# Performance work log

Hardware: AMD Instinct MI355X
Metric: run time of the kernel (lower is better)

The kernel has to match this reference:

```python
import jax, jax.numpy as jnp
import numpy as np

N, E, G = 50000, 400000, 64
IN_CH, HID, H, EDGE_DIM = 128, 64, 4, 4
NEG_SLOPE = 0.2


def setup_inputs() -> dict:
    key = jax.random.key(0)
    ks = list(jax.random.split(key, 40))
    kit = iter(ks)

    def rn(shape, scale=0.05):
        return jax.random.normal(next(kit), shape, dtype=jnp.float32) * scale

    inp = {
        "x": jax.random.normal(next(kit), (N, IN_CH), dtype=jnp.float32),
        "edge_attr": jax.random.uniform(next(kit), (E, 2), dtype=jnp.float32),
        "edge_index": jax.random.randint(next(kit), (2, E), 0, N),
        "batch": jnp.sort(jax.random.randint(next(kit), (N,), 0, G)),
    }
    # edge feature fusion MLPs
    inp["W_et"] = rn((1, EDGE_DIM // 2)); inp["b_et"] = jnp.zeros((EDGE_DIM // 2,), jnp.float32)
    inp["W_uw"] = rn((1, EDGE_DIM // 2)); inp["b_uw"] = jnp.zeros((EDGE_DIM // 2,), jnp.float32)
    inp["W_ua"] = rn((1, 1));             inp["b_ua"] = jnp.zeros((1,), jnp.float32)
    # two GATv2 layers
    for li, ic in ((0, IN_CH), (1, HID)):
        inp[f"Wl{li}"] = rn((ic, H * HID)); inp[f"bl{li}"] = jnp.zeros((H * HID,), jnp.float32)
        inp[f"Wr{li}"] = rn((ic, H * HID)); inp[f"br{li}"] = jnp.zeros((H * HID,), jnp.float32)
        inp[f"att{li}"] = rn((H, HID))
        inp[f"We{li}"] = rn((EDGE_DIM, H * HID))
        inp[f"bias{li}"] = jnp.zeros((HID,), jnp.float32)
    # heads
    inp["W_fc"] = rn((HID, HID)); inp["b_fc"] = jnp.zeros((HID,), jnp.float32)
    inp["W_res"] = rn((HID, 1)); inp["b_res"] = jnp.zeros((1,), jnp.float32)
    inp["W_time"] = rn((HID, 1)); inp["b_time"] = jnp.zeros((1,), jnp.float32)
    return inp


def gatv2_layer(x, src, dst, edge_attr_proj, Wl, bl, Wr, br, att, We, bias):
    # GATv2Conv, concat=False (mean over heads)
    xl = (x @ Wl + bl).reshape(-1, H, HID)   # [N,H,C] transformed source feats
    xr = (x @ Wr + br).reshape(-1, H, HID)   # [N,H,C] transformed target feats
    ee = (edge_attr_proj @ We).reshape(-1, H, HID)  # [E,H,C]
    xj = xl[src]                              # per-edge gather of source
    m = jax.nn.leaky_relu(xj + xr[dst] + ee, NEG_SLOPE)  # [E,H,C]
    score = jnp.einsum('ehc,hc->eh', m, att)  # [E,H]
    # segment softmax over incoming edges of each destination node
    smax = jax.ops.segment_max(score, dst, num_segments=N)  # [N,H]
    ex = jnp.exp(score - smax[dst])
    denom = jax.ops.segment_sum(ex, dst, num_segments=N)
    alpha = ex / (denom[dst] + 1e-16)         # [E,H]
    out = jax.ops.segment_sum(xj * alpha[..., None], dst, num_segments=N)  # [N,H,C]
    return out.mean(axis=1) + bias            # [N,C]


def reference(x, edge_attr, W_et, b_et, W_uw, b_uw, W_ua, b_ua,
              Wl0, bl0, Wr0, br0, att0, We0, bias0,
              Wl1, bl1, Wr1, br1, att1, We1, bias1,
              W_fc, b_fc, W_res, b_res, W_time, b_time,
              edge_index, batch):
    src, dst = edge_index[0], edge_index[1]
    edge_type = edge_attr[:, 0:1]
    unwind = edge_attr[:, 1:2]
    et_emb = edge_type @ W_et + b_et
    uw_emb = unwind @ W_uw + b_uw
    uw_att = jax.nn.sigmoid(unwind @ W_ua + b_ua)
    eap = jnp.concatenate([et_emb, uw_emb * uw_att], axis=-1)  # [E,4]

    h = jax.nn.relu(gatv2_layer(x, src, dst, eap, Wl0, bl0, Wr0, br0, att0, We0, bias0))
    h = jax.nn.relu(gatv2_layer(h, src, dst, eap, Wl1, bl1, Wr1, br1, att1, We1, bias1))

    # global mean pool over graphs (dropout is identity at inference)
    sums = jax.ops.segment_sum(h, batch, num_segments=G)
    cnts = jax.ops.segment_sum(jnp.ones((h.shape[0],), h.dtype), batch, num_segments=G)
    pooled = sums / jnp.maximum(cnts, 1.0)[:, None]
    g = jax.nn.relu(pooled @ W_fc + b_fc)
    result = g @ W_res + b_res
    time = g @ W_time + b_time
    return jnp.concatenate([result, time], axis=1)  # [G,2]
```

## Files before the change

kernel.cpp:

```cpp
#include <hip/hip_runtime.h>
#include <math.h>

namespace {

constexpr int N = 50000;
constexpr int E = 400000;
constexpr int G = 64;
constexpr int HID = 64;
constexpr int HH = 256;
constexpr int NCT = 32;
constexpr float NEG = 0.2f;

typedef __attribute__((ext_vector_type(8))) short short8v;
typedef __attribute__((ext_vector_type(4))) float f32x4;

__device__ __forceinline__ unsigned short f2bf(float f) {
    unsigned int u = __float_as_uint(f);
    u += 0x7FFFu + ((u >> 16) & 1u);
    return (unsigned short)(u >> 16);
}
__device__ __forceinline__ float bf2f(unsigned short h) {
    return __uint_as_float(((unsigned int)h) << 16);
}

__global__ __launch_bounds__(256) void hist_k(
    const int* __restrict__ dst, int* __restrict__ deg, int* __restrict__ rank)
{
    int e = blockIdx.x * 256 + threadIdx.x;
    if (e < E) rank[e] = atomicAdd(&deg[dst[e]], 1);
}

__global__ __launch_bounds__(256) void scan1_k(
    const int* __restrict__ deg, int* __restrict__ pre, int* __restrict__ bsum)
{
    __shared__ int s[256];
    int i = blockIdx.x * 256 + threadIdx.x;
    int v = (i < N) ? deg[i] : 0;
    s[threadIdx.x] = v;
    __syncthreads();
    for (int off = 1; off < 256; off <<= 1) {
        int t = (threadIdx.x >= off) ? s[threadIdx.x - off] : 0;
        __syncthreads();
        s[threadIdx.x] += t;
        __syncthreads();
    }
    if (i < N) pre[i] = s[threadIdx.x] - v;
    if (threadIdx.x == 255) bsum[blockIdx.x] = s[255];
}

__global__ __launch_bounds__(256) void scan2_k(int* __restrict__ bsum, int nb)
{
    __shared__ int s[256];
    int tid = threadIdx.x;
    int v = (tid < nb) ? bsum[tid] : 0;
    s[tid] = v;
    __syncthreads();
    for (int off = 1; off < 256; off <<= 1) {
        int t = (tid >= off) ? s[tid - off] : 0;
        __syncthreads();
        s[tid] += t;
        __syncthreads();
    }
    if (tid < nb) bsum[tid] = s[tid] - v;
}

__global__ __launch_bounds__(256) void scatter_k(
    const int* __restrict__ src, const int* __restrict__ dst,
    const float* __restrict__ ea,
    const float* __restrict__ W_et, const float* __restrict__ b_et,
    const float* __restrict__ W_uw, const float* __restrict__ b_uw,
    const float* __restrict__ W_ua, const float* __restrict__ b_ua,
    const int* __restrict__ pre, const int* __restrict__ bsum,
    const int* __restrict__ rank,
    int* __restrict__ csr_src, float* __restrict__ eap_csr)
{
    int e = blockIdx.x * 256 + threadIdx.x;
    if (e >= E) return;
    float et = ea[e * 2 + 0], uw = ea[e * 2 + 1];
    float ua = 1.f / (1.f + expf(-(uw * W_ua[0] + b_ua[0])));
    float4 v;
    v.x = et * W_et[0] + b_et[0];
    v.y = et * W_et[1] + b_et[1];
    v.z = (uw * W_uw[0] + b_uw[0]) * ua;
    v.w = (uw * W_uw[1] + b_uw[1]) * ua;
    int d = dst[e];
    int pos = pre[d] + bsum[d >> 8] + rank[e];
    csr_src[pos] = src[e];
    *(float4*)&eap_csr[(size_t)pos * 4] = v;
}

__global__ __launch_bounds__(256) void pack_k(
    const float* __restrict__ Wl0, const float* __restrict__ Wr0,
    const float* __restrict__ bl0, const float* __restrict__ br0,
    const float* __restrict__ Wl1, const float* __restrict__ Wr1,
    const float* __restrict__ bl1, const float* __restrict__ br1,
    unsigned short* __restrict__ w0hi, unsigned short* __restrict__ w0lo,
    unsigned short* __restrict__ w1hi, unsigned short* __restrict__ w1lo,
    float* __restrict__ bc0, float* __restrict__ bc1)
{
    int idx = blockIdx.x * 256 + threadIdx.x;
    if (idx < 8192) {
        int lane = idx & 63, ct = (idx >> 6) & 31, kt = idx >> 11;
        int col = ct * 16 + (lane & 15);
        const float* W = (col < 256) ? Wl0 : Wr0;
        int c = col & 255;
        int kb = kt * 32 + ((lane >> 4) & 3) * 8;
#pragma unroll
        for (int e = 0; e < 8; e++) {
            float v = W[(size_t)(kb + e) * 256 + c];
            unsigned short hi = f2bf(v);
            unsigned short lo = f2bf(v - bf2f(hi));
            w0hi[(size_t)idx * 8 + e] = hi;
            w0lo[(size_t)idx * 8 + e] = lo;
        }
    } else if (idx < 8192 + 4096) {
        int s = idx - 8192;
        int lane = s & 63, ct = (s >> 6) & 31, kt = s >> 11;
        int col = ct * 16 + (lane & 15);
        const float* W = (col < 256) ? Wl1 : Wr1;
        int c = col & 255;
        int kb = kt * 32 + ((lane >> 4) & 3) * 8;
#pragma unroll
        for (int e = 0; e < 8; e++) {
            float v = W[(size_t)(kb + e) * 256 + c];
            unsigned short hi = f2bf(v);
            unsigned short lo = f2bf(v - bf2f(hi));
            w1hi[(size_t)s * 8 + e] = hi;
            w1lo[(size_t)s * 8 + e] = lo;
        }
    } else if (idx < 8192 + 4096 + 512) {
        int i = idx - (8192 + 4096);
        bc0[i] = (i < 256) ? bl0[i] : br0[i - 256];
    } else if (idx < 8192 + 4096 + 1024) {
        int i = idx - (8192 + 4096 + 512);
        bc1[i] = (i < 256) ? bl1[i] : br1[i - 256];
    }
}

template <int IC>
__global__ __launch_bounds__(256) void projmm_k(
    const float* __restrict__ x,
    const unsigned short* __restrict__ whi, const unsigned short* __restrict__ wlo,
    const float* __restrict__ bc,
    float* __restrict__ xl, float* __restrict__ xr)
{
    constexpr int KT = IC / 32;
    constexpr int LDX = IC + 4;
    __shared__ float xs[32][LDX];
    const int base = blockIdx.x * 32;
    const int tid = threadIdx.x;
    for (int idx = tid; idx < 32 * IC / 4; idx += 256) {
        int j = idx / (IC / 4), k4 = idx - j * (IC / 4);
        int n = base + j;
        float4 v = make_float4(0.f, 0.f, 0.f, 0.f);
        if (n < N) v = *(const float4*)&x[(size_t)n * IC + k4 * 4];
        *(float4*)&xs[j][k4 * 4] = v;
    }
    __syncthreads();
    const int w = tid >> 6, lane = tid & 63;
    const int lr = lane & 15, lg = lane >> 4;
    f32x4 acc[2][8];
#pragma unroll
    for (int rt = 0; rt < 2; rt++)
#pragma unroll
        for (int ct = 0; ct < 8; ct++) {
            f32x4 z = {0.f, 0.f, 0.f, 0.f};
            acc[rt][ct] = z;
        }
#pragma unroll
    for (int kt = 0; kt < KT; kt++) {
        short8v ahi[2], alo[2];
#pragma unroll
        for (int rt = 0; rt < 2; rt++) {
            const float* p = &xs[rt * 16 + lr][kt * 32 + lg * 8];
            float4 v0 = *(const float4*)p;
            float4 v1 = *(const float4*)(p + 4);
            float fv[8] = {v0.x, v0.y, v0.z, v0.w, v1.x, v1.y, v1.z, v1.w};
            short8v h, l;
#pragma unroll
            for (int e = 0; e < 8; e++) {
                unsigned short hb = f2bf(fv[e]);
                h[e] = (short)hb;
                l[e] = (short)f2bf(fv[e] - bf2f(hb));
            }
            ahi[rt] = h;
            alo[rt] = l;
        }
        const size_t bbase = ((size_t)(kt * NCT + w * 8) * 64 + lane) * 8;
#pragma unroll
        for (int ct = 0; ct < 8; ct++) {
            short8v bhi = *(const short8v*)&whi[bbase + (size_t)ct * 64 * 8];
            short8v blo = *(const short8v*)&wlo[bbase + (size_t)ct * 64 * 8];
#pragma unroll
            for (int rt = 0; rt < 2; rt++) {
                acc[rt][ct] = __builtin_amdgcn_mfma_f32_16x16x32_bf16(ahi[rt], bhi, acc[rt][ct], 0, 0, 0);
                acc[rt][ct] = __builtin_amdgcn_mfma_f32_16x16x32_bf16(alo[rt], bhi, acc[rt][ct], 0, 0, 0);
                acc[rt][ct] = __builtin_amdgcn_mfma_f32_16x16x32_bf16(ahi[rt], blo, acc[rt][ct], 0, 0, 0);
            }
        }
    }
#pragma unroll
    for (int ct = 0; ct < 8; ct++) {
        int col = (w * 8 + ct) * 16 + lr;
        float bv = bc[col];
        float* target;
        int c;
        if (col < 256) { target = xl; c = col; }
        else           { target = xr; c = col - 256; }
#pragma unroll
        for (int rt = 0; rt < 2; rt++) {
            int row0 = base + rt * 16 + lg * 4;
            f32x4 a = acc[rt][ct];
#pragma unroll
            for (int i = 0; i < 4; i++) {
                int r = row0 + i;
                if (r < N) target[(size_t)r * HH + c] = a[i] + bv;
            }
        }
    }
}

__global__ __launch_bounds__(256) void gat_aggr_k(
    const float* __restrict__ xl, const float* __restrict__ xr,
    const float* __restrict__ eap_csr, const float* __restrict__ We,
    const float* __restrict__ att,
    const int* __restrict__ pre, const int* __restrict__ bsum,
    const int* __restrict__ deg,
    const int* __restrict__ csr_src,
    const float* __restrict__ bias, float* __restrict__ hout)
{
    int d = blockIdx.x * 4 + (threadIdx.x >> 6);
    int lane = threadIdx.x & 63;
    if (d >= N) return;
    int c4 = lane * 4;
    const float4 w0 = *(const float4*)&We[0 * HH + c4];
    const float4 w1 = *(const float4*)&We[1 * HH + c4];
    const float4 w2 = *(const float4*)&We[2 * HH + c4];
    const float4 w3 = *(const float4*)&We[3 * HH + c4];
    const float4 av = *(const float4*)&att[c4];
    const float4 vr = *(const float4*)&xr[(size_t)d * HH + c4];
    int start = pre[d] + bsum[d >> 8];
    int end = start + deg[d];
    float m = -INFINITY, denom = 0.f;
    float ax = 0.f, ay = 0.f, az = 0.f, aw = 0.f;
    int idx = start;
    for (; idx + 4 <= end; idx += 4) {
        int s0 = csr_src[idx], s1 = csr_src[idx + 1];
        int s2 = csr_src[idx + 2], s3 = csr_src[idx + 3];
        float4 a0 = *(const float4*)&eap_csr[(size_t)(idx + 0) * 4];
        float4 a1 = *(const float4*)&eap_csr[(size_t)(idx + 1) * 4];
        float4 a2 = *(const float4*)&eap_csr[(size_t)(idx + 2) * 4];
        float4 a3 = *(const float4*)&eap_csr[(size_t)(idx + 3) * 4];
        float4 vl0 = *(const float4*)&xl[(size_t)s0 * HH + c4];
        float4 vl1 = *(const float4*)&xl[(size_t)s1 * HH + c4];
        float4 vl2 = *(const float4*)&xl[(size_t)s2 * HH + c4];
        float4 vl3 = *(const float4*)&xl[(size_t)s3 * HH + c4];
        float p0, p1, p2, p3;
        {
            float q0 = vl0.x + vr.x + a0.x * w0.x + a0.y * w1.x + a0.z * w2.x + a0.w * w3.x;
            float q1 = vl0.y + vr.y + a0.x * w0.y + a0.y * w1.y + a0.z * w2.y + a0.w * w3.y;
            float q2 = vl0.z + vr.z + a0.x * w0.z + a0.y * w1.z + a0.z * w2.z + a0.w * w3.z;
            float q3 = vl0.w + vr.w + a0.x * w0.w + a0.y * w1.w + a0.z * w2.w + a0.w * w3.w;
            q0 = (q0 > 0.f) ? q0 : NEG * q0; q1 = (q1 > 0.f) ? q1 : NEG * q1;
            q2 = (q2 > 0.f) ? q2 : NEG * q2; q3 = (q3 > 0.f) ? q3 : NEG * q3;
            p0 = q0 * av.x + q1 * av.y + q2 * av.z + q3 * av.w;
        }
        {
            float q0 = vl1.x + vr.x + a1.x * w0.x + a1.y * w1.x + a1.z * w2.x + a1.w * w3.x;
            float q1 = vl1.y + vr.y + a1.x * w0.y + a1.y * w1.y + a1.z * w2.y + a1.w * w3.y;
            float q2 = vl1.z + vr.z + a1.x * w0.z + a1.y * w1.z + a1.z * w2.z + a1.w * w3.z;
            float q3 = vl1.w + vr.w + a1.x * w0.w + a1.y * w1.w + a1.z * w2.w + a1.w * w3.w;
            q0 = (q0 > 0.f) ? q0 : NEG * q0; q1 = (q1 > 0.f) ? q1 : NEG * q1;
            q2 = (q2 > 0.f) ? q2 : NEG * q2; q3 = (q3 > 0.f) ? q3 : NEG * q3;
            p1 = q0 * av.x + q1 * av.y + q2 * av.z + q3 * av.w;
        }
        {
            float q0 = vl2.x + vr.x + a2.x * w0.x + a2.y * w1.x + a2.z * w2.x + a2.w * w3.x;
            float q1 = vl2.y + vr.y + a2.x * w0.y + a2.y * w1.y + a2.z * w2.y + a2.w * w3.y;
            float q2 = vl2.z + vr.z + a2.x * w0.z + a2.y * w1.z + a2.z * w2.z + a2.w * w3.z;
            float q3 = vl2.w + vr.w + a2.x * w0.w + a2.y * w1.w + a2.z * w2.w + a2.w * w3.w;
            q0 = (q0 > 0.f) ? q0 : NEG * q0; q1 = (q1 > 0.f) ? q1 : NEG * q1;
            q2 = (q2 > 0.f) ? q2 : NEG * q2; q3 = (q3 > 0.f) ? q3 : NEG * q3;
            p2 = q0 * av.x + q1 * av.y + q2 * av.z + q3 * av.w;
        }
        {
            float q0 = vl3.x + vr.x + a3.x * w0.x + a3.y * w1.x + a3.z * w2.x + a3.w * w3.x;
            float q1 = vl3.y + vr.y + a3.x * w0.y + a3.y * w1.y + a3.z * w2.y + a3.w * w3.y;
            float q2 = vl3.z + vr.z + a3.x * w0.z + a3.y * w1.z + a3.z * w2.z + a3.w * w3.z;
            float q3 = vl3.w + vr.w + a3.x * w0.w + a3.y * w1.w + a3.z * w2.w + a3.w * w3.w;
            q0 = (q0 > 0.f) ? q0 : NEG * q0; q1 = (q1 > 0.f) ? q1 : NEG * q1;
            q2 = (q2 > 0.f) ? q2 : NEG * q2; q3 = (q3 > 0.f) ? q3 : NEG * q3;
            p3 = q0 * av.x + q1 * av.y + q2 * av.z + q3 * av.w;
        }
#pragma unroll
        for (int off = 1; off <= 8; off <<= 1) {
            p0 += __shfl_xor(p0, off, 64);
            p1 += __shfl_xor(p1, off, 64);
            p2 += __shfl_xor(p2, off, 64);
            p3 += __shfl_xor(p3, off, 64);
        }
        float pm = fmaxf(fmaxf(p0, p1), fmaxf(p2, p3));
        float newm = fmaxf(m, pm);
        float so = expf(m - newm);
        float e0 = expf(p0 - newm);
        float e1 = expf(p1 - newm);
        float e2 = expf(p2 - newm);
        float e3 = expf(p3 - newm);
        denom = denom * so + e0 + e1 + e2 + e3;
        ax = ax * so + e0 * vl0.x + e1 * vl1.x + e2 * vl2.x + e3 * vl3.x;
        ay = ay * so + e0 * vl0.y + e1 * vl1.y + e2 * vl2.y + e3 * vl3.y;
        az = az * so + e0 * vl0.z + e1 * vl1.z + e2 * vl2.z + e3 * vl3.z;
        aw = aw * so + e0 * vl0.w + e1 * vl1.w + e2 * vl2.w + e3 * vl3.w;
        m = newm;
    }
    for (; idx < end; ++idx) {
        int s = csr_src[idx];
        float4 a = *(const float4*)&eap_csr[(size_t)idx * 4];
        float4 vl = *(const float4*)&xl[(size_t)s * HH + c4];
        float q0 = vl.x + vr.x + a.x * w0.x + a.y * w1.x + a.z * w2.x + a.w * w3.x;
        float q1 = vl.y + vr.y + a.x * w0.y + a.y * w1.y + a.z * w2.y + a.w * w3.y;
        float q2 = vl.z + vr.z + a.x * w0.z + a.y * w1.z + a.z * w2.z + a.w * w3.z;
        float q3 = vl.w + vr.w + a.x * w0.w + a.y * w1.w + a.z * w2.w + a.w * w3.w;
        q0 = (q0 > 0.f) ? q0 : NEG * q0; q1 = (q1 > 0.f) ? q1 : NEG * q1;
        q2 = (q2 > 0.f) ? q2 : NEG * q2; q3 = (q3 > 0.f) ? q3 : NEG * q3;
        float p = q0 * av.x + q1 * av.y + q2 * av.z + q3 * av.w;
#pragma unroll
        for (int off = 1; off <= 8; off <<= 1) p += __shfl_xor(p, off, 64);
        float newm = fmaxf(m, p);
        float so = expf(m - newm);
        float ex = expf(p - newm);
        denom = denom * so + ex;
        ax = ax * so + ex * vl.x;
        ay = ay * so + ex * vl.y;
        az = az * so + ex * vl.z;
        aw = aw * so + ex * vl.w;
        m = newm;
    }
    float inv = 0.25f / (denom + 1e-16f);
    ax *= inv; ay *= inv; az *= inv; aw *= inv;
    ax += __shfl_xor(ax, 16, 64); ax += __shfl_xor(ax, 32, 64);
    ay += __shfl_xor(ay, 16, 64); ay += __shfl_xor(ay, 32, 64);
    az += __shfl_xor(az, 16, 64); az += __shfl_xor(az, 32, 64);
    aw += __shfl_xor(aw, 16, 64); aw += __shfl_xor(aw, 32, 64);
    if (lane < 16) {
        float4 b = *(const float4*)&bias[c4];
        float4 o;
        o.x = fmaxf(ax + b.x, 0.f);
        o.y = fmaxf(ay + b.y, 0.f);
        o.z = fmaxf(az + b.z, 0.f);
        o.w = fmaxf(aw + b.w, 0.f);
        *(float4*)&hout[(size_t)d * HID + c4] = o;
    }
}

__global__ __launch_bounds__(256) void pool_k(
    const float* __restrict__ h, const int* __restrict__ batch,
    float* __restrict__ pooled)
{
    constexpr int CH = 16;
    int c = threadIdx.x & 63;
    int chunk = blockIdx.x * 4 + (threadIdx.x >> 6);
    int n0 = chunk * CH;
    if (n0 >= N) return;
    int nend = (n0 + CH < N) ? n0 + CH : N;
    float sum = 0.f;
    int curb = batch[n0];
    for (int n = n0; n < nend; ++n) {
        int b = batch[n];
        if (b != curb) {
            atomicAdd(&pooled[curb * HID + c], sum);
            sum = 0.f; curb = b;
        }
        sum += h[(size_t)n * HID + c];
    }
    atomicAdd(&pooled[curb * HID + c], sum);
}

__global__ __launch_bounds__(64) void head_k(
    const float* __restrict__ pooled, const int* __restrict__ batch,
    const float* __restrict__ W_fc, const float* __restrict__ b_fc,
    const float* __restrict__ W_res, const float* __restrict__ b_res,
    const float* __restrict__ W_time, const float* __restrict__ b_time,
    float* __restrict__ out)
{
    int g = blockIdx.x;
    int c = threadIdx.x;
    int lo = 0, hi = N;
    while (lo < hi) { int mid = (lo + hi) >> 1; if (batch[mid] < g) lo = mid + 1; else hi = mid; }
    int start = lo;
    hi = N;
    while (lo < hi) { int mid = (lo + hi) >> 1; if (batch[mid] < g + 1) lo = mid + 1; else hi = mid; }
    int end = lo;
    float cnt = (float)(end - start);
    float p = pooled[g * HID + c] / fmaxf(cnt, 1.0f);
    __shared__ float ps[HID];
    ps[c] = p;
    __syncthreads();
    float gv = b_fc[c];
    for (int k = 0; k < HID; k++) gv += ps[k] * W_fc[k * HID + c];
    gv = fmaxf(gv, 0.f);
    float r = gv * W_res[c];
    float t = gv * W_time[c];
#pragma unroll
    for (int off = 32; off > 0; off >>= 1) {
        r += __shfl_down(r, off, 64);
        t += __shfl_down(t, off, 64);
    }
    if (c == 0) {
        out[g * 2 + 0] = r + b_res[0];
        out[g * 2 + 1] = t + b_time[0];
    }
}

}

extern "C" void kernel_launch(void* const* d_in, const int* in_sizes, int n_in,
                              void* d_out, int out_size, void* d_ws, size_t ws_size,
                              hipStream_t stream) {
    const float* x         = (const float*)d_in[0];
    const float* edge_attr = (const float*)d_in[1];
    const int*   edge_index= (const int*)d_in[2];
    const int*   batch     = (const int*)d_in[3];
    const float* W_et = (const float*)d_in[4];
    const float* b_et = (const float*)d_in[5];
    const float* W_uw = (const float*)d_in[6];
    const float* b_uw = (const float*)d_in[7];
    const float* W_ua = (const float*)d_in[8];
    const float* b_ua = (const float*)d_in[9];
    const float* Wl0  = (const float*)d_in[10];
    const float* bl0  = (const float*)d_in[11];
    const float* Wr0  = (const float*)d_in[12];
    const float* br0  = (const float*)d_in[13];
    const float* att0 = (const float*)d_in[14];
    const float* We0  = (const float*)d_in[15];
    const float* bias0= (const float*)d_in[16];
    const float* Wl1  = (const float*)d_in[17];
    const float* bl1  = (const float*)d_in[18];
    const float* Wr1  = (const float*)d_in[19];
    const float* br1  = (const float*)d_in[20];
    const float* att1 = (const float*)d_in[21];
    const float* We1  = (const float*)d_in[22];
    const float* bias1= (const float*)d_in[23];
    const float* W_fc = (const float*)d_in[24];
    const float* b_fc = (const float*)d_in[25];
    const float* W_res= (const float*)d_in[26];
    const float* b_res= (const float*)d_in[27];
    const float* W_time=(const float*)d_in[28];
    const float* b_time=(const float*)d_in[29];

    const int* src = edge_index;
    const int* dst = edge_index + E;

    float* ws    = (float*)d_ws;
    float* xl    = ws;
    float* xr    = xl  + (size_t)N * HH;
    float* h1    = xr  + (size_t)N * HH;
    float* h2    = h1  + (size_t)N * HID;
    float* pooled= h2  + (size_t)N * HID;
    int*   deg      = (int*)(pooled + (size_t)G * HID);
    int*   pre      = deg + N;
    int*   bsum     = pre + N;
    int*   rank     = bsum + 256;
    int*   csr_src  = rank + E;
    float* eap_csr  = (float*)(csr_src + E);
    unsigned short* w0hi = (unsigned short*)rank;
    unsigned short* w0lo = w0hi + 65536;
    unsigned short* w1hi = w0lo + 65536;
    unsigned short* w1lo = w1hi + 32768;
    float* bc0 = (float*)(w1lo + 32768);
    float* bc1 = bc0 + 512;

    dim3 b256(256);
    const int NB = (N + 255) / 256;
    const int NPROJ = (N + 31) / 32;

    hipMemsetAsync(pooled, 0, (size_t)(G * HID + N) * 4, stream);
    hist_k<<<(E + 255) / 256, b256, 0, stream>>>(dst, deg, rank);
    scan1_k<<<NB, b256, 0, stream>>>(deg, pre, bsum);
    scan2_k<<<1, b256, 0, stream>>>(bsum, NB);
    scatter_k<<<(E + 255) / 256, b256, 0, stream>>>(
        src, dst, edge_attr, W_et, b_et, W_uw, b_uw, W_ua, b_ua,
        pre, bsum, rank, csr_src, eap_csr);
    pack_k<<<52, b256, 0, stream>>>(Wl0, Wr0, bl0, br0, Wl1, Wr1, bl1, br1,
                                    w0hi, w0lo, w1hi, w1lo, bc0, bc1);

    projmm_k<128><<<NPROJ, b256, 0, stream>>>(x, w0hi, w0lo, bc0, xl, xr);
    gat_aggr_k<<<(N + 3) / 4, b256, 0, stream>>>(
        xl, xr, eap_csr, We0, att0, pre, bsum, deg, csr_src, bias0, h1);

    projmm_k<64><<<NPROJ, b256, 0, stream>>>(h1, w1hi, w1lo, bc1, xl, xr);
    gat_aggr_k<<<(N + 3) / 4, b256, 0, stream>>>(
        xl, xr, eap_csr, We1, att1, pre, bsum, deg, csr_src, bias1, h2);

    pool_k<<<((N + 15) / 16 + 3) / 4, b256, 0, stream>>>(h2, batch, pooled);
    head_k<<<G, dim3(64), 0, stream>>>(
        pooled, batch, W_fc, b_fc, W_res, b_res, W_time, b_time, (float*)d_out);
}
```

Before: 421.0 us.

## Store projected features as bf16 and use persistent atomic work queue in aggregation

```diff
diff --git a/kernel.cpp b/kernel.cpp
--- a/kernel.cpp
+++ b/kernel.cpp
@@ -10,6 +10,7 @@
 constexpr int HH = 256;
 constexpr int NCT = 32;
 constexpr float NEG = 0.2f;
+constexpr int GAT_BLOCKS = 2048;
 
 typedef __attribute__((ext_vector_type(8))) short short8v;
 typedef __attribute__((ext_vector_type(4))) float f32x4;
@@ -21,6 +22,15 @@
 }
 __device__ __forceinline__ float bf2f(unsigned short h) {
     return __uint_as_float(((unsigned int)h) << 16);
+}
+__device__ __forceinline__ float4 ld_bf4(const unsigned short* p) {
+    uint2 u = *(const uint2*)p;
+    float4 r;
+    r.x = __uint_as_float(u.x << 16);
+    r.y = __uint_as_float(u.x & 0xFFFF0000u);
+    r.z = __uint_as_float(u.y << 16);
+    r.w = __uint_as_float(u.y & 0xFFFF0000u);
+    return r;
 }
 
 __global__ __launch_bounds__(256) void hist_k(
@@ -96,9 +106,11 @@
     const float* __restrict__ bl1, const float* __restrict__ br1,
     unsigned short* __restrict__ w0hi, unsigned short* __restrict__ w0lo,
     unsigned short* __restrict__ w1hi, unsigned short* __restrict__ w1lo,
-    float* __restrict__ bc0, float* __restrict__ bc1)
+    float* __restrict__ bc0, float* __restrict__ bc1,
+    int* __restrict__ ctr)
 {
     int idx = blockIdx.x * 256 + threadIdx.x;
+    if (idx == 0) { ctr[0] = 0; ctr[1] = 0; }
     if (idx < 8192) {
         int lane = idx & 63, ct = (idx >> 6) & 31, kt = idx >> 11;
         int col = ct * 16 + (lane & 15);
@@ -142,7 +154,7 @@
     const float* __restrict__ x,
     const unsigned short* __restrict__ whi, const unsigned short* __restrict__ wlo,
     const float* __restrict__ bc,
-    float* __restrict__ xl, float* __restrict__ xr)
+    unsigned short* __restrict__ xlb, unsigned short* __restrict__ xrb)
 {
     constexpr int KT = IC / 32;
     constexpr int LDX = IC + 4;
@@ -203,10 +215,10 @@
     for (int ct = 0; ct < 8; ct++) {
         int col = (w * 8 + ct) * 16 + lr;
         float bv = bc[col];
-        float* target;
+        unsigned short* target;
         int c;
-        if (col < 256) { target = xl; c = col; }
-        else           { target = xr; c = col - 256; }
+        if (col < 256) { target = xlb; c = col; }
+        else           { target = xrb; c = col - 256; }
 #pragma unroll
         for (int rt = 0; rt < 2; rt++) {
             int row0 = base + rt * 16 + lg * 4;
@@ -214,142 +226,152 @@
 #pragma unroll
             for (int i = 0; i < 4; i++) {
                 int r = row0 + i;
-                if (r < N) target[(size_t)r * HH + c] = a[i] + bv;
+                if (r < N) target[(size_t)r * HH + c] = f2bf(a[i] + bv);
             }
         }
     }
 }
 
 __global__ __launch_bounds__(256) void gat_aggr_k(
-    const float* __restrict__ xl, const float* __restrict__ xr,
+    const unsigned short* __restrict__ xlb, const unsigned short* __restrict__ xrb,
     const float* __restrict__ eap_csr, const float* __restrict__ We,
     const float* __restrict__ att,
     const int* __restrict__ pre, const int* __restrict__ bsum,
     const int* __restrict__ deg,
     const int* __restrict__ csr_src,
-    const float* __restrict__ bias, float* __restrict__ hout)
-{
-    int d = blockIdx.x * 4 + (threadIdx.x >> 6);
-    int lane = threadIdx.x & 63;
-    if (d >= N) return;
-    int c4 = lane * 4;
+    const float* __restrict__ bias, float* __restrict__ hout,
+    int* __restrict__ ctr)
+{
+    const int lane = threadIdx.x & 63;
+    const int c4 = lane * 4;
     const float4 w0 = *(const float4*)&We[0 * HH + c4];
     const float4 w1 = *(const float4*)&We[1 * HH + c4];
     const float4 w2 = *(const float4*)&We[2 * HH + c4];
     const float4 w3 = *(const float4*)&We[3 * HH + c4];
     const float4 av = *(const float4*)&att[c4];
-    const float4 vr = *(const float4*)&xr[(size_t)d * HH + c4];
-    int start = pre[d] + bsum[d >> 8];
-    int end = start + deg[d];
-    float m = -INFINITY, denom = 0.f;
-    float ax = 0.f, ay = 0.f, az = 0.f, aw = 0.f;
-    int idx = start;
-    for (; idx + 4 <= end; idx += 4) {
-        int s0 = csr_src[idx], s1 = csr_src[idx + 1];
-        int s2 = csr_src[idx + 2], s3 = csr_src[idx + 3];
-        float4 a0 = *(const float4*)&eap_csr[(size_t)(idx + 0) * 4];
-        float4 a1 = *(const float4*)&eap_csr[(size_t)(idx + 1) * 4];
-        float4 a2 = *(const float4*)&eap_csr[(size_t)(idx + 2) * 4];
-        float4 a3 = *(const float4*)&eap_csr[(size_t)(idx + 3) * 4];
-        float4 vl0 = *(const float4*)&xl[(size_t)s0 * HH + c4];
-        float4 vl1 = *(const float4*)&xl[(size_t)s1 * HH + c4];
-        float4 vl2 = *(const float4*)&xl[(size_t)s2 * HH + c4];
-        float4 vl3 = *(const float4*)&xl[(size_t)s3 * HH + c4];
-        float p0, p1, p2, p3;
-        {
-            float q0 = vl0.x + vr.x + a0.x * w0.x + a0.y * w1.x + a0.z * w2.x + a0.w * w3.x;
-            float q1 = vl0.y + vr.y + a0.x * w0.y + a0.y * w1.y + a0.z * w2.y + a0.w * w3.y;
-            float q2 = vl0.z + vr.z + a0.x * w0.z + a0.y * w1.z + a0.z * w2.z + a0.w * w3.z;
-            float q3 = vl0.w + vr.w + a0.x * w0.w + a0.y * w1.w + a0.z * w2.w + a0.w * w3.w;
+    float4 bb = make_float4(0.f, 0.f, 0.f, 0.f);
+    if (lane < 16) bb = *(const float4*)&bias[c4];
+
+    int draw = 0;
+    if (lane == 0) draw = atomicAdd(ctr, 1);
+    int d = __builtin_amdgcn_readfirstlane(draw);
+    while (d < N) {
+        int dnraw = 0;
+        if (lane == 0) dnraw = atomicAdd(ctr, 1);
+
+        int start = pre[d] + bsum[d >> 8];
+        int end = start + deg[d];
+        const float4 vr = ld_bf4(&xrb[(size_t)d * HH + c4]);
+        float m = -INFINITY, denom = 0.f;
+        float ax = 0.f, ay = 0.f, az = 0.f, aw = 0.f;
+        int idx = start;
+        for (; idx + 4 <= end; idx += 4) {
+            int s0 = csr_src[idx], s1 = csr_src[idx + 1];
+            int s2 = csr_src[idx + 2], s3 = csr_src[idx + 3];
+            float4 a0 = *(const float4*)&eap_csr[(size_t)(idx + 0) * 4];
+            float4 a1 = *(const float4*)&eap_csr[(size_t)(idx + 1) * 4];
+            float4 a2 = *(const float4*)&eap_csr[(size_t)(idx + 2) * 4];
+            float4 a3 = *(const float4*)&eap_csr[(size_t)(idx + 3) * 4];
+            float4 vl0 = ld_bf4(&xlb[(size_t)s0 * HH + c4]);
+            float4 vl1 = ld_bf4(&xlb[(size_t)s1 * HH + c4]);
+            float4 vl2 = ld_bf4(&xlb[(size_t)s2 * HH + c4]);
+            float4 vl3 = ld_bf4(&xlb[(size_t)s3 * HH + c4]);
+            float p0, p1, p2, p3;
+            {
+                float q0 = vl0.x + vr.x + a0.x * w0.x + a0.y * w1.x + a0.z * w2.x + a0.w * w3.x;
+                float q1 = vl0.y + vr.y + a0.x * w0.y + a0.y * w1.y + a0.z * w2.y + a0.w * w3.y;
+                float q2 = vl0.z + vr.z + a0.x * w0.z + a0.y * w1.z + a0.z * w2.z + a0.w * w3.z;
+                float q3 = vl0.w + vr.w + a0.x * w0.w + a0.y * w1.w + a0.z * w2.w + a0.w * w3.w;
+                q0 = (q0 > 0.f) ? q0 : NEG * q0; q1 = (q1 > 0.f) ? q1 : NEG * q1;
+                q2 = (q2 > 0.f) ? q2 : NEG * q2; q3 = (q3 > 0.f) ? q3 : NEG * q3;
+                p0 = q0 * av.x + q1 * av.y + q2 * av.z + q3 * av.w;
+            }
+            {
+                float q0 = vl1.x + vr.x + a1.x * w0.x + a1.y * w1.x + a1.z * w2.x + a1.w * w3.x;
+                float q1 = vl1.y + vr.y + a1.x * w0.y + a1.y * w1.y + a1.z * w2.y + a1.w * w3.y;
+                float q2 = vl1.z + vr.z + a1.x * w0.z + a1.y * w1.z + a1.z * w2.z + a1.w * w3.z;
+                float q3 = vl1.w + vr.w + a1.x * w0.w + a1.y * w1.w + a1.z * w2.w + a1.w * w3.w;
+                q0 = (q0 > 0.f) ? q0 : NEG * q0; q1 = (q1 > 0.f) ? q1 : NEG * q1;
+                q2 = (q2 > 0.f) ? q2 : NEG * q2; q3 = (q3 > 0.f) ? q3 : NEG * q3;
+                p1 = q0 * av.x + q1 * av.y + q2 * av.z + q3 * av.w;
+            }
+            {
+                float q0 = vl2.x + vr.x + a2.x * w0.x + a2.y * w1.x + a2.z * w2.x + a2.w * w3.x;
+                float q1 = vl2.y + vr.y + a2.x * w0.y + a2.y * w1.y + a2.z * w2.y + a2.w * w3.y;
+                float q2 = vl2.z + vr.z + a2.x * w0.z + a2.y * w1.z + a2.z * w2.z + a2.w * w3.z;
+                float q3 = vl2.w + vr.w + a2.x * w0.w + a2.y * w1.w + a2.z * w2.w + a2.w * w3.w;
+                q0 = (q0 > 0.f) ? q0 : NEG * q0; q1 = (q1 > 0.f) ? q1 : NEG * q1;
+                q2 = (q2 > 0.f) ? q2 : NEG * q2; q3 = (q3 > 0.f) ? q3 : NEG * q3;
+                p2 = q0 * av.x + q1 * av.y + q2 * av.z + q3 * av.w;
+            }
+            {
+                float q0 = vl3.x + vr.x + a3.x * w0.x + a3.y * w1.x + a3.z * w2.x + a3.w * w3.x;
+                float q1 = vl3.y + vr.y + a3.x * w0.y + a3.y * w1.y + a3.z * w2.y + a3.w * w3.y;
+                float q2 = vl3.z + vr.z + a3.x * w0.z + a3.y * w1.z + a3.z * w2.z + a3.w * w3.z;
+                float q3 = vl3.w + vr.w + a3.x * w0.w + a3.y * w1.w + a3.z * w2.w + a3.w * w3.w;
+                q0 = (q0 > 0.f) ? q0 : NEG * q0; q1 = (q1 > 0.f) ? q1 : NEG * q1;
+                q2 = (q2 > 0.f) ? q2 : NEG * q2; q3 = (q3 > 0.f) ? q3 : NEG * q3;
+                p3 = q0 * av.x + q1 * av.y + q2 * av.z + q3 * av.w;
+            }
+#pragma unroll
+            for (int off = 1; off <= 8; off <<= 1) {
+                p0 += __shfl_xor(p0, off, 64);
+                p1 += __shfl_xor(p1, off, 64);
+                p2 += __shfl_xor(p2, off, 64);
+                p3 += __shfl_xor(p3, off, 64);
+            }
+            float pm = fmaxf(fmaxf(p0, p1), fmaxf(p2, p3));
+            float newm = fmaxf(m, pm);
+            float so = expf(m - newm);
+            float e0 = expf(p0 - newm);
+            float e1 = expf(p1 - newm);
+            float e2 = expf(p2 - newm);
+            float e3 = expf(p3 - newm);
+            denom = denom * so + e0 + e1 + e2 + e3;
+            ax = ax * so + e0 * vl0.x + e1 * vl1.x + e2 * vl2.x + e3 * vl3.x;
+            ay = ay * so + e0 * vl0.y + e1 * vl1.y + e2 * vl2.y + e3 * vl3.y;
+            az = az * so + e0 * vl0.z + e1 * vl1.z + e2 * vl2.z + e3 * vl3.z;
+            aw = aw * so + e0 * vl0.w + e1 * vl1.w + e2 * vl2.w + e3 * vl3.w;
+            m = newm;
+        }
+        for (; idx < end; ++idx) {
+            int s = csr_src[idx];
+            float4 a = *(const float4*)&eap_csr[(size_t)idx * 4];
+            float4 vl = ld_bf4(&xlb[(size_t)s * HH + c4]);
+            float q0 = vl.x + vr.x + a.x * w0.x + a.y * w1.x + a.z * w2.x + a.w * w3.x;
+            float q1 = vl.y + vr.y + a.x * w0.y + a.y * w1.y + a.z * w2.y + a.w * w3.y;
+            float q2 = vl.z + vr.z + a.x * w0.z + a.y * w1.z + a.z * w2.z + a.w * w3.z;
+            float q3 = vl.w + vr.w + a.x * w0.w + a.y * w1.w + a.z * w2.w + a.w * w3.w;
             q0 = (q0 > 0.f) ? q0 : NEG * q0; q1 = (q1 > 0.f) ? q1 : NEG * q1;
             q2 = (q2 > 0.f) ? q2 : NEG * q2; q3 = (q3 > 0.f) ? q3 : NEG * q3;
-            p0 = q0 * av.x + q1 * av.y + q2 * av.z + q3 * av.w;
-        }
-        {
-            float q0 = vl1.x + vr.x + a1.x * w0.x + a1.y * w1.x + a1.z * w2.x + a1.w * w3.x;
-            float q1 = vl1.y + vr.y + a1.x * w0.y + a1.y * w1.y + a1.z * w2.y + a1.w * w3.y;
-            float q2 = vl1.z + vr.z + a1.x * w0.z + a1.y * w1.z + a1.z * w2.z + a1.w * w3.z;
-            float q3 = vl1.w + vr.w + a1.x * w0.w + a1.y * w1.w + a1.z * w2.w + a1.w * w3.w;
-            q0 = (q0 > 0.f) ? q0 : NEG * q0; q1 = (q1 > 0.f) ? q1 : NEG * q1;
-            q2 = (q2 > 0.f) ? q2 : NEG * q2; q3 = (q3 > 0.f) ? q3 : NEG * q3;
-            p1 = q0 * av.x + q1 * av.y + q2 * av.z + q3 * av.w;
-        }
-        {
-            float q0 = vl2.x + vr.x + a2.x * w0.x + a2.y * w1.x + a2.z * w2.x + a2.w * w3.x;
-            float q1 = vl2.y + vr.y + a2.x * w0.y + a2.y * w1.y + a2.z * w2.y + a2.w * w3.y;
-            float q2 = vl2.z + vr.z + a2.x * w0.z + a2.y * w1.z + a2.z * w2.z + a2.w * w3.z;
-            float q3 = vl2.w + vr.w + a2.x * w0.w + a2.y * w1.w + a2.z * w2.w + a2.w * w3.w;
-            q0 = (q0 > 0.f) ? q0 : NEG * q0; q1 = (q1 > 0.f) ? q1 : NEG * q1;
-            q2 = (q2 > 0.f) ? q2 : NEG * q2; q3 = (q3 > 0.f) ? q3 : NEG * q3;
-            p2 = q0 * av.x + q1 * av.y + q2 * av.z + q3 * av.w;
-        }
-        {
-            float q0 = vl3.x + vr.x + a3.x * w0.x + a3.y * w1.x + a3.z * w2.x + a3.w * w3.x;
-            float q1 = vl3.y + vr.y + a3.x * w0.y + a3.y * w1.y + a3.z * w2.y + a3.w * w3.y;
-            float q2 = vl3.z + vr.z + a3.x * w0.z + a3.y * w1.z + a3.z * w2.z + a3.w * w3.z;
-            float q3 = vl3.w + vr.w + a3.x * w0.w + a3.y * w1.w + a3.z * w2.w + a3.w * w3.w;
-            q0 = (q0 > 0.f) ? q0 : NEG * q0; q1 = (q1 > 0.f) ? q1 : NEG * q1;
-            q2 = (q2 > 0.f) ? q2 : NEG * q2; q3 = (q3 > 0.f) ? q3 : NEG * q3;
-            p3 = q0 * av.x + q1 * av.y + q2 * av.z + q3 * av.w;
-        }
-#pragma unroll
-        for (int off = 1; off <= 8; off <<= 1) {
-            p0 += __shfl_xor(p0, off, 64);
-            p1 += __shfl_xor(p1, off, 64);
-            p2 += __shfl_xor(p2, off, 64);
-            p3 += __shfl_xor(p3, off, 64);
-        }
-        float pm = fmaxf(fmaxf(p0, p1), fmaxf(p2, p3));
-        float newm = fmaxf(m, pm);
-        float so = expf(m - newm);
-        float e0 = expf(p0 - newm);
-        float e1 = expf(p1 - newm);
-        float e2 = expf(p2 - newm);
-        float e3 = expf(p3 - newm);
-        denom = denom * so + e0 + e1 + e2 + e3;
-        ax = ax * so + e0 * vl0.x + e1 * vl1.x + e2 * vl2.x + e3 * vl3.x;
-        ay = ay * so + e0 * vl0.y + e1 * vl1.y + e2 * vl2.y + e3 * vl3.y;
-        az = az * so + e0 * vl0.z + e1 * vl1.z + e2 * vl2.z + e3 * vl3.z;
-        aw = aw * so + e0 * vl0.w + e1 * vl1.w + e2 * vl2.w + e3 * vl3.w;
-        m = newm;
-    }
-    for (; idx < end; ++idx) {
-        int s = csr_src[idx];
-        float4 a = *(const float4*)&eap_csr[(size_t)idx * 4];
-        float4 vl = *(const float4*)&xl[(size_t)s * HH + c4];
-        float q0 = vl.x + vr.x + a.x * w0.x + a.y * w1.x + a.z * w2.x + a.w * w3.x;
-        float q1 = vl.y + vr.y + a.x * w0.y + a.y * w1.y + a.z * w2.y + a.w * w3.y;
-        float q2 = vl.z + vr.z + a.x * w0.z + a.y * w1.z + a.z * w2.z + a.w * w3.z;
-        float q3 = vl.w + vr.w + a.x * w0.w + a.y * w1.w + a.z * w2.w + a.w * w3.w;
-        q0 = (q0 > 0.f) ? q0 : NEG * q0; q1 = (q1 > 0.f) ? q1 : NEG * q1;
-        q2 = (q2 > 0.f) ? q2 : NEG * q2; q3 = (q3 > 0.f) ? q3 : NEG * q3;
-        float p = q0 * av.x + q1 * av.y + q2 * av.z + q3 * av.w;
-#pragma unroll
-        for (int off = 1; off <= 8; off <<= 1) p += __shfl_xor(p, off, 64);
-        float newm = fmaxf(m, p);
-        float so = expf(m - newm);
-        float ex = expf(p - newm);
-        denom = denom * so + ex;
-        ax = ax * so + ex * vl.x;
-        ay = ay * so + ex * vl.y;
-        az = az * so + ex * vl.z;
-        aw = aw * so + ex * vl.w;
-        m = newm;
-    }
-    float inv = 0.25f / (denom + 1e-16f);
-    ax *= inv; ay *= inv; az *= inv; aw *= inv;
-    ax += __shfl_xor(ax, 16, 64); ax += __shfl_xor(ax, 32, 64);
-    ay += __shfl_xor(ay, 16, 64); ay += __shfl_xor(ay, 32, 64);
-    az += __shfl_xor(az, 16, 64); az += __shfl_xor(az, 32, 64);
-    aw += __shfl_xor(aw, 16, 64); aw += __shfl_xor(aw, 32, 64);
-    if (lane < 16) {
-        float4 b = *(const float4*)&bias[c4];
-        float4 o;
-        o.x = fmaxf(ax + b.x, 0.f);
-        o.y = fmaxf(ay + b.y, 0.f);
-        o.z = fmaxf(az + b.z, 0.f);
-        o.w = fmaxf(aw + b.w, 0.f);
-        *(float4*)&hout[(size_t)d * HID + c4] = o;
+            float p = q0 * av.x + q1 * av.y + q2 * av.z + q3 * av.w;
+#pragma unroll
+            for (int off = 1; off <= 8; off <<= 1) p += __shfl_xor(p, off, 64);
+            float newm = fmaxf(m, p);
+            float so = expf(m - newm);
+            float ex = expf(p - newm);
+            denom = denom * so + ex;
+            ax = ax * so + ex * vl.x;
+            ay = ay * so + ex * vl.y;
+            az = az * so + ex * vl.z;
+            aw = aw * so + ex * vl.w;
+            m = newm;
+        }
+        float inv = 0.25f / (denom + 1e-16f);
+        ax *= inv; ay *= inv; az *= inv; aw *= inv;
+        ax += __shfl_xor(ax, 16, 64); ax += __shfl_xor(ax, 32, 64);
+        ay += __shfl_xor(ay, 16, 64); ay += __shfl_xor(ay, 32, 64);
+        az += __shfl_xor(az, 16, 64); az += __shfl_xor(az, 32, 64);
+        aw += __shfl_xor(aw, 16, 64); aw += __shfl_xor(aw, 32, 64);
+        if (lane < 16) {
+            float4 o;
+            o.x = fmaxf(ax + bb.x, 0.f);
+            o.y = fmaxf(ay + bb.y, 0.f);
+            o.z = fmaxf(az + bb.z, 0.f);
+            o.w = fmaxf(aw + bb.w, 0.f);
+            *(float4*)&hout[(size_t)d * HID + c4] = o;
+        }
+        d = __builtin_amdgcn_readfirstlane(dnraw);
     }
 }
 
@@ -452,9 +474,9 @@
     const int* dst = edge_index + E;
 
     float* ws    = (float*)d_ws;
-    float* xl    = ws;
-    float* xr    = xl  + (size_t)N * HH;
-    float* h1    = xr  + (size_t)N * HH;
+    unsigned short* xlb = (unsigned short*)ws;
+    unsigned short* xrb = (unsigned short*)(ws + (size_t)N * HH);
+    float* h1    = ws  + (size_t)2 * N * HH;
     float* h2    = h1  + (size_t)N * HID;
     float* pooled= h2  + (size_t)N * HID;
     int*   deg      = (int*)(pooled + (size_t)G * HID);
@@ -469,6 +491,7 @@
     unsigned short* w1lo = w1hi + 32768;
     float* bc0 = (float*)(w1lo + 32768);
     float* bc1 = bc0 + 512;
+    int*   ctr = (int*)(bc1 + 512);
 
     dim3 b256(256);
     const int NB = (N + 255) / 256;
@@ -482,15 +505,15 @@
         src, dst, edge_attr, W_et, b_et, W_uw, b_uw, W_ua, b_ua,
         pre, bsum, rank, csr_src, eap_csr);
     pack_k<<<52, b256, 0, stream>>>(Wl0, Wr0, bl0, br0, Wl1, Wr1, bl1, br1,
-                                    w0hi, w0lo, w1hi, w1lo, bc0, bc1);
-
-    projmm_k<128><<<NPROJ, b256, 0, stream>>>(x, w0hi, w0lo, bc0, xl, xr);
-    gat_aggr_k<<<(N + 3) / 4, b256, 0, stream>>>(
-        xl, xr, eap_csr, We0, att0, pre, bsum, deg, csr_src, bias0, h1);
-
-    projmm_k<64><<<NPROJ, b256, 0, stream>>>(h1, w1hi, w1lo, bc1, xl, xr);
-    gat_aggr_k<<<(N + 3) / 4, b256, 0, stream>>>(
-        xl, xr, eap_csr, We1, att1, pre, bsum, deg, csr_src, bias1, h2);
+                                    w0hi, w0lo, w1hi, w1lo, bc0, bc1, ctr);
+
+    projmm_k<128><<<NPROJ, b256, 0, stream>>>(x, w0hi, w0lo, bc0, xlb, xrb);
+    gat_aggr_k<<<GAT_BLOCKS, b256, 0, stream>>>(
+        xlb, xrb, eap_csr, We0, att0, pre, bsum, deg, csr_src, bias0, h1, ctr + 0);
+
+    projmm_k<64><<<NPROJ, b256, 0, stream>>>(h1, w1hi, w1lo, bc1, xlb, xrb);
+    gat_aggr_k<<<GAT_BLOCKS, b256, 0, stream>>>(
+        xlb, xrb, eap_csr, We1, att1, pre, bsum, deg, csr_src, bias1, h2, ctr + 1);
 
     pool_k<<<((N + 15) / 16 + 3) / 4, b256, 0, stream>>>(h2, batch, pooled);
     head_k<<<G, dim3(64), 0, stream>>>(
```

Result: slower. 1.620 ms (+284.9%).
